# Performance work log

Hardware: AMD Instinct MI355X
Metric: run time of the kernel (lower is better)

The kernel has to match this reference:

```python
import jax, jax.numpy as jnp
import numpy as np

B, N, L, H, HE, EO = 16, 256, 64, 32, 128, 64
NUM_MPS = 3
ALPHA = 0.2


def _lrelu(x):
    return jnp.where(x >= 0, x, ALPHA * x)


def setup_inputs() -> dict:
    key = jax.random.key(0)
    ks = jax.random.split(key, 8)
    rn = lambda k, sh, s=0.05: jax.random.normal(k, sh, dtype=jnp.float32) * s
    return {
        "x": rn(ks[0], (B, L), 1.0),
        "W_lin": rn(ks[1], (L, N * L)),
        "b_lin": jnp.zeros((N * L,), jnp.float32),
        "W_in": rn(ks[2], (L, H)),
        "b_in": jnp.zeros((H,), jnp.float32),
        "We1": rn(ks[3], (NUM_MPS, 2 * H, HE)),
        "be1": jnp.zeros((NUM_MPS, HE), jnp.float32),
        "We2": rn(ks[4], (NUM_MPS, HE, EO)),
        "be2": jnp.zeros((NUM_MPS, EO), jnp.float32),
        "Wn0": rn(ks[5], (NUM_MPS, H + EO, H)),
        "bn0": jnp.zeros((NUM_MPS, H), jnp.float32),
        "Wn1": rn(ks[6], (NUM_MPS, H, H)),
        "bn1": jnp.zeros((NUM_MPS, H), jnp.float32),
    }


def _graphnet(h, We1, be1, We2, be2, Wn0, bn0, Wn1, bn1):
    # h: [B, N, H]; fully connected graph, NUM_MPS message passing rounds.
    for t in range(NUM_MPS):
        W1 = We1[t]
        # edge input is concat(h_i, h_j); split the first edge-layer matmul so
        # the [B,N,N,2H] concat is never materialized.
        rcv = jnp.einsum('bnh,hk->bnk', h, W1[:H])   # receiver contribution
        snd = jnp.einsum('bnh,hk->bnk', h, W1[H:])   # sender contribution
        e = _lrelu(rcv[:, :, None, :] + snd[:, None, :, :] + be1[t])  # [B,N,N,HE]
        e = _lrelu(jnp.einsum('bijk,ko->bijo', e, We2[t]) + be2[t])   # [B,N,N,EO]
        m = e.sum(axis=2)                                              # [B,N,EO] sum-aggregate over senders
        n = jnp.concatenate([h, m], axis=-1)                           # [B,N,H+EO]
        n = _lrelu(jnp.einsum('bnf,fh->bnh', n, Wn0[t]) + bn0[t])
        h = _lrelu(jnp.einsum('bnh,hk->bnk', n, Wn1[t]) + bn1[t])
    return h


def reference(x, W_lin, b_lin, W_in, b_in, We1, be1, We2, be2, Wn0, bn0, Wn1, bn1):
    bsz = x.shape[0]
    h = (x @ W_lin + b_lin).reshape(bsz, N, L)  # latent -> per-node latent features
    h = h @ W_in + b_in                          # project to hidden/output node size
    h = _graphnet(h, We1, be1, We2, be2, Wn0, bn0, Wn1, bn1)
    return jnp.tanh(h)                           # [B, N, node_size]
```

## Files before the change

### kernel.cpp

```cpp
#include <hip/hip_runtime.h>
#include <hip/hip_bf16.h>

#define B_  16
#define N_  256
#define L_  64
#define H_  32
#define HE_ 128
#define EO_ 64

typedef __attribute__((ext_vector_type(8))) short bf16x8;
typedef __attribute__((ext_vector_type(4))) float f32x4;

__device__ __forceinline__ unsigned cvt_pk_bf16(float a, float b) {
  unsigned r;
  asm("v_cvt_pk_bf16_f32 %0, %1, %2" : "=v"(r) : "v"(a), "v"(b));
  return r;
}

__global__ void k_setup(const float* __restrict__ We1, const float* __restrict__ be1,
                        const float* __restrict__ We2, const float* __restrict__ be2,
                        float* __restrict__ Wp, float* __restrict__ Wq,
                        float* __restrict__ bp, uint4* __restrict__ Bfrag) {
  const int t   = blockIdx.y;
  const int gid = blockIdx.x * 256 + threadIdx.x;
  const float* We1t = We1 + t * 64 * 128;
  const float* We2t = We2 + t * 128 * 64;

  {
    int f = gid >> 6, o = gid & 63;
    float ap = 0.f, aq = 0.f;
    for (int k = 0; k < 128; ++k) {
      float w2 = We2t[k * 64 + o];
      ap += We1t[f * 128 + k] * w2;
      aq += We1t[(32 + f) * 128 + k] * w2;
    }
    Wp[(t * 32 + f) * 64 + o] = 0.6f * ap;
    Wq[(t * 32 + f) * 64 + o] = 0.6f * aq;
  }
  if (gid < 64) {
    float ab = be2[t * 64 + gid];
    for (int k = 0; k < 128; ++k) ab += 0.6f * be1[t * 128 + k] * We2t[k * 64 + gid];
    bp[t * 64 + gid] = ab;
  }
  if (gid < 1024) {
    int u = gid;
    int kk = u >> 8, nt = (u >> 6) & 3, ln = u & 63;
    int k0 = kk * 32 + (ln >> 4) * 8, o = nt * 16 + (ln & 15);
    unsigned w[4];
#pragma unroll
    for (int p = 0; p < 4; ++p) {
      float v0 = 0.4f * We2t[(k0 + 2 * p) * 64 + o];
      float v1 = 0.4f * We2t[(k0 + 2 * p + 1) * 64 + o];
      w[p] = cvt_pk_bf16(v0, v1);
    }
    Bfrag[t * 1024 + u] = make_uint4(w[0], w[1], w[2], w[3]);
  }
}

__global__ __launch_bounds__(256) void k_init(const float* __restrict__ x,
                                              const float* __restrict__ W_lin,
                                              const float* __restrict__ b_lin,
                                              const float* __restrict__ W_in,
                                              const float* __restrict__ b_in,
                                              float* __restrict__ h) {
  __shared__ float sm[4][64];
  const int w = threadIdx.x >> 6, lane = threadIdx.x & 63;
  const int row = __builtin_amdgcn_readfirstlane(blockIdx.x * 4 + w);
  const int b = row >> 8, n = row & 255;
  float acc = b_lin[n * 64 + lane];
  const float* xb = x + b * 64;
  for (int l = 0; l < 64; ++l)
    acc += xb[l] * W_lin[l * (N_ * L_) + n * 64 + lane];
  sm[w][lane] = acc;
  __syncthreads();
  if (lane < 32) {
    float hacc = b_in[lane];
#pragma unroll 8
    for (int f = 0; f < 64; ++f) hacc += sm[w][f] * W_in[f * 32 + lane];
    h[row * 32 + lane] = hacc;
  }
}

__global__ __launch_bounds__(256) void k_proj(const float* __restrict__ h,
                                              const float* __restrict__ We1,
                                              const float* __restrict__ be1,
                                              const float* __restrict__ Wp,
                                              const float* __restrict__ Wq,
                                              const float* __restrict__ bp,
                                              float* __restrict__ Rp, float* __restrict__ S,
                                              float* __restrict__ P, float* __restrict__ Q,
                                              int t) {
  const int lane = threadIdx.x & 63;
  const int row = __builtin_amdgcn_readfirstlane(blockIdx.x * 4 + (threadIdx.x >> 6));
  const float* hr = h + row * 32;
  const float* We1t = We1 + t * 64 * 128;
  float r0 = be1[t * 128 + lane], r1 = be1[t * 128 + 64 + lane];
  float s0 = 0.f, s1 = 0.f;
  float p = bp[t * 64 + lane], q = 0.f;
  for (int f = 0; f < 32; ++f) {
    float hf = hr[f];
    r0 += hf * We1t[f * 128 + lane];
    r1 += hf * We1t[f * 128 + 64 + lane];
    s0 += hf * We1t[(32 + f) * 128 + lane];
    s1 += hf * We1t[(32 + f) * 128 + 64 + lane];
    p  += hf * Wp[(t * 32 + f) * 64 + lane];
    q  += hf * Wq[(t * 32 + f) * 64 + lane];
  }
  Rp[row * 128 + lane] = r0;  Rp[row * 128 + 64 + lane] = r1;
  S [row * 128 + lane] = s0;  S [row * 128 + 64 + lane] = s1;
  P [row * 64 + lane]  = p;   Q [row * 64 + lane]       = q;
}

template <bool LAST>
__global__ __launch_bounds__(512, 2) void k_edge(
    const float* __restrict__ Rp, const float* __restrict__ S,
    const float* __restrict__ P, const float* __restrict__ Q,
    const uint4* __restrict__ Bfrag,
    const float* __restrict__ Wn0, const float* __restrict__ bn0,
    const float* __restrict__ Wn1, const float* __restrict__ bn1,
    float* __restrict__ h_io, float* __restrict__ out, int t) {
  const int b  = blockIdx.y;
  const int i0 = blockIdx.x * 16;
  const int tid = threadIdx.x;
  const int w = tid >> 6, lane = tid & 63;
  const int col = lane & 15, kg = lane >> 4;

  __shared__ float h_tile[16 * 33];
  __shared__ float mred[8 * 1040];
  __shared__ float mfin[16 * 65];
  __shared__ float n_lds[16 * 33];

  {
    int il = tid >> 5, o = tid & 31;
    h_tile[il * 33 + o] = h_io[((b << 8) + i0 + il) * 32 + o];
  }

  union BU { uint4 q; bf16x8 v; };
  BU bfr[4][4];
#pragma unroll
  for (int kk = 0; kk < 4; ++kk)
#pragma unroll
    for (int nt = 0; nt < 4; ++nt)
      bfr[kk][nt].q = Bfrag[((t * 4 + kk) * 4 + nt) * 64 + lane];

  float4 rA[4][2];
  const float* rB = Rp + (size_t)((b << 8) + i0 + col) * 128 + kg * 8;
#pragma unroll
  for (int kk = 0; kk < 4; ++kk) {
    rA[kk][0] = *(const float4*)(rB + kk * 32);
    rA[kk][1] = *(const float4*)(rB + kk * 32 + 4);
  }

  float pb[4][4];
#pragma unroll
  for (int nt = 0; nt < 4; ++nt)
#pragma unroll
    for (int r = 0; r < 4; ++r)
      pb[nt][r] = P[(size_t)((b << 8) + i0 + kg * 4 + r) * 64 + nt * 16 + col];

  float m[4][4] = {};
  const float* sB = S + (size_t)(b << 8) * 128 + kg * 8;
  const float* qB = Q + (size_t)(b << 8) * 64 + col;

  const int j0 = w * 32;
  for (int j = j0; j < j0 + 32; ++j) {
    const float* sj = sB + (size_t)j * 128;
    float qv[4];
#pragma unroll
    for (int nt = 0; nt < 4; ++nt) qv[nt] = qB[(size_t)j * 64 + nt * 16];

    BU af[4];
#pragma unroll
    for (int kk = 0; kk < 4; ++kk) {
      float4 s0 = *(const float4*)(sj + kk * 32);
      float4 s1 = *(const float4*)(sj + kk * 32 + 4);
      float4 r0 = rA[kk][0], r1 = rA[kk][1];
      unsigned u0 = cvt_pk_bf16(fabsf(r0.x + s0.x), fabsf(r0.y + s0.y));
      unsigned u1 = cvt_pk_bf16(fabsf(r0.z + s0.z), fabsf(r0.w + s0.w));
      unsigned u2 = cvt_pk_bf16(fabsf(r1.x + s1.x), fabsf(r1.y + s1.y));
      unsigned u3 = cvt_pk_bf16(fabsf(r1.z + s1.z), fabsf(r1.w + s1.w));
      af[kk].q = make_uint4(u0, u1, u2, u3);
    }

    f32x4 acc[4];
#pragma unroll
    for (int nt = 0; nt < 4; ++nt) {
      float q = qv[nt];
      f32x4 c;
      c[0] = pb[nt][0] + q; c[1] = pb[nt][1] + q;
      c[2] = pb[nt][2] + q; c[3] = pb[nt][3] + q;
      acc[nt] = c;
    }
#pragma unroll
    for (int kk = 0; kk < 4; ++kk)
#pragma unroll
      for (int nt = 0; nt < 4; ++nt)
        acc[nt] = __builtin_amdgcn_mfma_f32_16x16x32_bf16(af[kk].v, bfr[kk][nt].v, acc[nt], 0, 0, 0);

#pragma unroll
    for (int nt = 0; nt < 4; ++nt)
#pragma unroll
      for (int r = 0; r < 4; ++r) {
        float e = acc[nt][r];
        m[nt][r] += fmaxf(e, 0.2f * e);
      }
  }

#pragma unroll
  for (int nt = 0; nt < 4; ++nt)
#pragma unroll
    for (int r = 0; r < 4; ++r)
      mred[w * 1040 + (kg * 4 + r) * 65 + nt * 16 + col] = m[nt][r];
  __syncthreads();

  for (int e = tid; e < 1024; e += 512) {
    int il = e >> 6, o = e & 63;
    float s = 0.f;
#pragma unroll
    for (int w2 = 0; w2 < 8; ++w2) s += mred[w2 * 1040 + il * 65 + o];
    mfin[il * 65 + o] = s;
  }
  __syncthreads();

  {
    int il = tid >> 5, o = tid & 31;
    float a0 = bn0[t * 32 + o];
    const float* w0 = Wn0 + (size_t)t * 96 * 32 + o;
#pragma unroll 8
    for (int f = 0; f < 32; ++f) a0 += h_tile[il * 33 + f] * w0[f * 32];
#pragma unroll 8
    for (int f = 0; f < 64; ++f) a0 += mfin[il * 65 + f] * w0[(32 + f) * 32];
    a0 = fmaxf(a0, 0.2f * a0);
    n_lds[il * 33 + o] = a0;
  }
  __syncthreads();

  {
    int il = tid >> 5, o = tid & 31;
    float a1 = bn1[t * 32 + o];
    const float* w1 = Wn1 + (size_t)t * 32 * 32 + o;
#pragma unroll 8
    for (int f = 0; f < 32; ++f) a1 += n_lds[il * 33 + f] * w1[f * 32];
    a1 = fmaxf(a1, 0.2f * a1);
    int gi = ((b << 8) + i0 + il) * 32 + o;
    if (LAST) out[gi] = tanhf(a1);
    else      h_io[gi] = a1;
  }
}

extern "C" void kernel_launch(void* const* d_in, const int* in_sizes, int n_in,
                              void* d_out, int out_size, void* d_ws, size_t ws_size,
                              hipStream_t stream) {
  const float* x     = (const float*)d_in[0];
  const float* W_lin = (const float*)d_in[1];
  const float* b_lin = (const float*)d_in[2];
  const float* W_in  = (const float*)d_in[3];
  const float* b_in  = (const float*)d_in[4];
  const float* We1   = (const float*)d_in[5];
  const float* be1   = (const float*)d_in[6];
  const float* We2   = (const float*)d_in[7];
  const float* be2   = (const float*)d_in[8];
  const float* Wn0   = (const float*)d_in[9];
  const float* bn0   = (const float*)d_in[10];
  const float* Wn1   = (const float*)d_in[11];
  const float* bn1   = (const float*)d_in[12];
  float* out = (float*)d_out;

  float* ws = (float*)d_ws;
  float* h  = ws;
  float* Rp = ws + 131072;
  float* Sb = ws + 655360;
  float* Pb = ws + 1179648;
  float* Qb = ws + 1441792;
  float* Wp = ws + 1703936;
  float* Wq = ws + 1710080;
  float* bp = ws + 1716224;
  uint4* Bf = (uint4*)(ws + 1716416);

  k_setup<<<dim3(8, 3), 256, 0, stream>>>(We1, be1, We2, be2, Wp, Wq, bp, Bf);
  k_init<<<1024, 256, 0, stream>>>(x, W_lin, b_lin, W_in, b_in, h);
  for (int t = 0; t < 3; ++t) {
    k_proj<<<1024, 256, 0, stream>>>(h, We1, be1, Wp, Wq, bp, Rp, Sb, Pb, Qb, t);
    if (t < 2)
      k_edge<false><<<dim3(16, 16), 512, 0, stream>>>(Rp, Sb, Pb, Qb, Bf,
                                                      Wn0, bn0, Wn1, bn1, h, nullptr, t);
    else
      k_edge<true><<<dim3(16, 16), 512, 0, stream>>>(Rp, Sb, Pb, Qb, Bf,
                                                     Wn0, bn0, Wn1, bn1, h, out, t);
  }
}
```

Measured before the change: 241.2 us.

## Split edge kernel over sender chunks and move node MLP to separate kernel

Splits the edge-message kernel across four sender chunks via a third grid dimension, using 256-thread blocks, so 1024 blocks run instead of 256 and the GPU is better filled. Partial message sums go to a workspace buffer, and a new node kernel adds the four partials and runs the node MLP. Also folds the abs into the bf16 convert instruction's source modifier and rewrites leaky-ReLU accumulation as two FMAs. In exchange it adds an extra launch per round and a global round trip for the partial sums.

```diff
diff --git a/kernel.cpp b/kernel.cpp
--- a/kernel.cpp
+++ b/kernel.cpp
@@ -14,6 +14,11 @@
 __device__ __forceinline__ unsigned cvt_pk_bf16(float a, float b) {
   unsigned r;
   asm("v_cvt_pk_bf16_f32 %0, %1, %2" : "=v"(r) : "v"(a), "v"(b));
+  return r;
+}
+__device__ __forceinline__ unsigned cvt_pk_bf16_abs(float a, float b) {
+  unsigned r;
+  asm("v_cvt_pk_bf16_f32 %0, |%1|, |%2|" : "=v"(r) : "v"(a), "v"(b));
   return r;
 }
 
@@ -111,29 +116,18 @@
   P [row * 64 + lane]  = p;   Q [row * 64 + lane]       = q;
 }
 
-template <bool LAST>
-__global__ __launch_bounds__(512, 2) void k_edge(
+__global__ __launch_bounds__(256, 4) void k_edge(
     const float* __restrict__ Rp, const float* __restrict__ S,
     const float* __restrict__ P, const float* __restrict__ Q,
-    const uint4* __restrict__ Bfrag,
-    const float* __restrict__ Wn0, const float* __restrict__ bn0,
-    const float* __restrict__ Wn1, const float* __restrict__ bn1,
-    float* __restrict__ h_io, float* __restrict__ out, int t) {
+    const uint4* __restrict__ Bfrag, float* __restrict__ m_part, int t) {
   const int b  = blockIdx.y;
   const int i0 = blockIdx.x * 16;
+  const int jb = blockIdx.z;
   const int tid = threadIdx.x;
   const int w = tid >> 6, lane = tid & 63;
   const int col = lane & 15, kg = lane >> 4;
 
-  __shared__ float h_tile[16 * 33];
-  __shared__ float mred[8 * 1040];
-  __shared__ float mfin[16 * 65];
-  __shared__ float n_lds[16 * 33];
-
-  {
-    int il = tid >> 5, o = tid & 31;
-    h_tile[il * 33 + o] = h_io[((b << 8) + i0 + il) * 32 + o];
-  }
+  __shared__ float mred[4 * 1040];
 
   union BU { uint4 q; bf16x8 v; };
   BU bfr[4][4];
@@ -162,8 +156,8 @@
   const float* sB = S + (size_t)(b << 8) * 128 + kg * 8;
   const float* qB = Q + (size_t)(b << 8) * 64 + col;
 
-  const int j0 = w * 32;
-  for (int j = j0; j < j0 + 32; ++j) {
+  const int j0 = jb * 64 + w * 16;
+  for (int j = j0; j < j0 + 16; ++j) {
     const float* sj = sB + (size_t)j * 128;
     float qv[4];
 #pragma unroll
@@ -175,10 +169,10 @@
       float4 s0 = *(const float4*)(sj + kk * 32);
       float4 s1 = *(const float4*)(sj + kk * 32 + 4);
       float4 r0 = rA[kk][0], r1 = rA[kk][1];
-      unsigned u0 = cvt_pk_bf16(fabsf(r0.x + s0.x), fabsf(r0.y + s0.y));
-      unsigned u1 = cvt_pk_bf16(fabsf(r0.z + s0.z), fabsf(r0.w + s0.w));
-      unsigned u2 = cvt_pk_bf16(fabsf(r1.x + s1.x), fabsf(r1.y + s1.y));
-      unsigned u3 = cvt_pk_bf16(fabsf(r1.z + s1.z), fabsf(r1.w + s1.w));
+      unsigned u0 = cvt_pk_bf16_abs(r0.x + s0.x, r0.y + s0.y);
+      unsigned u1 = cvt_pk_bf16_abs(r0.z + s0.z, r0.w + s0.w);
+      unsigned u2 = cvt_pk_bf16_abs(r1.x + s1.x, r1.y + s1.y);
+      unsigned u3 = cvt_pk_bf16_abs(r1.z + s1.z, r1.w + s1.w);
       af[kk].q = make_uint4(u0, u1, u2, u3);
     }
 
@@ -202,7 +196,7 @@
 #pragma unroll
       for (int r = 0; r < 4; ++r) {
         float e = acc[nt][r];
-        m[nt][r] += fmaxf(e, 0.2f * e);
+        m[nt][r] = fmaf(0.4f, fabsf(e), fmaf(0.6f, e, m[nt][r]));
       }
   }
 
@@ -213,39 +207,54 @@
       mred[w * 1040 + (kg * 4 + r) * 65 + nt * 16 + col] = m[nt][r];
   __syncthreads();
 
-  for (int e = tid; e < 1024; e += 512) {
+  for (int e = tid; e < 1024; e += 256) {
     int il = e >> 6, o = e & 63;
-    float s = 0.f;
-#pragma unroll
-    for (int w2 = 0; w2 < 8; ++w2) s += mred[w2 * 1040 + il * 65 + o];
-    mfin[il * 65 + o] = s;
+    float s = mred[il * 65 + o] + mred[1040 + il * 65 + o] +
+              mred[2080 + il * 65 + o] + mred[3120 + il * 65 + o];
+    m_part[(((size_t)jb * 16 + b) * 256 + i0 + il) * 64 + o] = s;
+  }
+}
+
+template <bool LAST>
+__global__ __launch_bounds__(256) void k_node(
+    const float* __restrict__ m_part,
+    const float* __restrict__ Wn0, const float* __restrict__ bn0,
+    const float* __restrict__ Wn1, const float* __restrict__ bn1,
+    float* __restrict__ h_io, float* __restrict__ out, int t) {
+  const int row0 = blockIdx.x * 8;
+  const int tid = threadIdx.x;
+  const int r = tid >> 5, o = tid & 31;
+  __shared__ float h_t[8][33];
+  __shared__ float mfin[8][65];
+  __shared__ float n_l[8][33];
+
+  h_t[r][o] = h_io[(row0 + r) * 32 + o];
+  for (int e = tid; e < 512; e += 256) {
+    int rr = e >> 6, oo = e & 63;
+    size_t base = (size_t)(row0 + rr) * 64 + oo;
+    mfin[rr][oo] = m_part[base] + m_part[base + 262144] +
+                   m_part[base + 524288] + m_part[base + 786432];
   }
   __syncthreads();
 
-  {
-    int il = tid >> 5, o = tid & 31;
-    float a0 = bn0[t * 32 + o];
-    const float* w0 = Wn0 + (size_t)t * 96 * 32 + o;
+  float a0 = bn0[t * 32 + o];
+  const float* w0 = Wn0 + (size_t)t * 96 * 32 + o;
 #pragma unroll 8
-    for (int f = 0; f < 32; ++f) a0 += h_tile[il * 33 + f] * w0[f * 32];
+  for (int f = 0; f < 32; ++f) a0 += h_t[r][f] * w0[f * 32];
 #pragma unroll 8
-    for (int f = 0; f < 64; ++f) a0 += mfin[il * 65 + f] * w0[(32 + f) * 32];
-    a0 = fmaxf(a0, 0.2f * a0);
-    n_lds[il * 33 + o] = a0;
-  }
+  for (int f = 0; f < 64; ++f) a0 += mfin[r][f] * w0[(32 + f) * 32];
+  a0 = fmaxf(a0, 0.2f * a0);
+  n_l[r][o] = a0;
   __syncthreads();
 
-  {
-    int il = tid >> 5, o = tid & 31;
-    float a1 = bn1[t * 32 + o];
-    const float* w1 = Wn1 + (size_t)t * 32 * 32 + o;
+  float a1 = bn1[t * 32 + o];
+  const float* w1 = Wn1 + (size_t)t * 1024 + o;
 #pragma unroll 8
-    for (int f = 0; f < 32; ++f) a1 += n_lds[il * 33 + f] * w1[f * 32];
-    a1 = fmaxf(a1, 0.2f * a1);
-    int gi = ((b << 8) + i0 + il) * 32 + o;
-    if (LAST) out[gi] = tanhf(a1);
-    else      h_io[gi] = a1;
-  }
+  for (int f = 0; f < 32; ++f) a1 += n_l[r][f] * w1[f * 32];
+  a1 = fmaxf(a1, 0.2f * a1);
+  int gi = (row0 + r) * 32 + o;
+  if (LAST) out[gi] = tanhf(a1);
+  else      h_io[gi] = a1;
 }
 
 extern "C" void kernel_launch(void* const* d_in, const int* in_sizes, int n_in,
@@ -272,20 +281,20 @@
   float* Sb = ws + 655360;
   float* Pb = ws + 1179648;
   float* Qb = ws + 1441792;
-  float* Wp = ws + 1703936;
-  float* Wq = ws + 1710080;
-  float* bp = ws + 1716224;
-  uint4* Bf = (uint4*)(ws + 1716416);
+  float* Mp = ws + 1703936;
+  float* Wp = ws + 2752512;
+  float* Wq = ws + 2758656;
+  float* bp = ws + 2764800;
+  uint4* Bf = (uint4*)(ws + 2764992);
 
   k_setup<<<dim3(8, 3), 256, 0, stream>>>(We1, be1, We2, be2, Wp, Wq, bp, Bf);
   k_init<<<1024, 256, 0, stream>>>(x, W_lin, b_lin, W_in, b_in, h);
   for (int t = 0; t < 3; ++t) {
     k_proj<<<1024, 256, 0, stream>>>(h, We1, be1, Wp, Wq, bp, Rp, Sb, Pb, Qb, t);
+    k_edge<<<dim3(16, 16, 4), 256, 0, stream>>>(Rp, Sb, Pb, Qb, Bf, Mp, t);
     if (t < 2)
-      k_edge<false><<<dim3(16, 16), 512, 0, stream>>>(Rp, Sb, Pb, Qb, Bf,
-                                                      Wn0, bn0, Wn1, bn1, h, nullptr, t);
+      k_node<false><<<512, 256, 0, stream>>>(Mp, Wn0, bn0, Wn1, bn1, h, nullptr, t);
     else
-      k_edge<true><<<dim3(16, 16), 512, 0, stream>>>(Rp, Sb, Pb, Qb, Bf,
-                                                     Wn0, bn0, Wn1, bn1, h, out, t);
-  }
-}
+      k_node<true><<<512, 256, 0, stream>>>(Mp, Wn0, bn0, Wn1, bn1, h, out, t);
+  }
+}
```

Result: slower. 410.7 us (+70.3%).
